# Optimization experiments

Measured on AMD Instinct MI355X. Metric: run time of the kernel, lower is better.

## Reference

```python
import jax, jax.numpy as jnp
import numpy as np

D = 128          # hidden_dim
H = 4            # num attention heads (torch default nhead=4 in this module)
DH = D // H
NA = 4096        # author nodes
NP = 100000      # paper nodes
EAP = 500000     # author->paper edges
EPA = 500000     # paper->author edges
DFF = 2048       # TransformerEncoderLayer FFN dim (torch default)
OUT = 16
IN_A = 128
IN_P = 256
EPS = 1e-5


def layer_norm(x, g, b):
    mu = jnp.mean(x, -1, keepdims=True)
    var = jnp.mean((x - mu) ** 2, -1, keepdims=True)
    return (x - mu) / jnp.sqrt(var + EPS) * g + b


def scatter_mean(vals, idx, n):
    # torch_scatter 'mean': empty segments yield 0
    s = jax.ops.segment_sum(vals, idx, num_segments=n)
    c = jax.ops.segment_sum(jnp.ones((vals.shape[0], 1), vals.dtype), idx, num_segments=n)
    return s / jnp.maximum(c, 1.0)


def metapath_layer(x_src, x_dst, src, dst, Wv, bv, Wo, bo, g, b):
    # nn.MultiheadAttention applied per-edge with seq_len=1 (query/key/value are
    # [1, E, D]); softmax over a single key is identically 1, so the attention
    # output is exactly out_proj(v_proj(x_src[src])) -- q/k projections have no
    # effect on the output (and zero gradient).
    v = x_src[src] @ Wv.T + bv            # [E, D] gather + value projection
    attn = v @ Wo.T + bo                  # output projection
    agg = scatter_mean(attn, dst, x_dst.shape[0])
    return layer_norm(agg + x_dst, g, b)


def fusion_layer(x, Wqkv, bqkv, Wo, bo, W1, b1, W2, b2, g1, bt1, g2, bt2):
    # torch TransformerEncoderLayer defaults: post-norm, relu, batch_first=False,
    # so x: [S=NA (seq), M (batch = #metapaths), D].
    S, M, _ = x.shape
    qkv = x @ Wqkv.T + bqkv               # [S, M, 3D]
    q, k, v = jnp.split(qkv, 3, axis=-1)
    q = q.reshape(S, M, H, DH)
    k = k.reshape(S, M, H, DH)
    v = v.reshape(S, M, H, DH)
    scores = jnp.einsum('smhd,tmhd->mhst', q, k) / np.float32(np.sqrt(DH))
    a = jax.nn.softmax(scores, axis=-1)
    ctx = jnp.einsum('mhst,tmhd->smhd', a, v).reshape(S, M, D)
    x = layer_norm(x + ctx @ Wo.T + bo, g1, bt1)
    ff = jax.nn.relu(x @ W1.T + b1) @ W2.T + b2
    return layer_norm(x + ff, g2, bt2)


def setup_inputs() -> dict:
    key = jax.random.key(0)
    ks = iter(jax.random.split(key, 64))
    def nrm(shape, scale=0.02):
        return jax.random.normal(next(ks), shape, dtype=jnp.float32) * scale
    inp = {
        'x_author': jax.random.normal(next(ks), (NA, IN_A), dtype=jnp.float32),
        'x_paper': jax.random.normal(next(ks), (NP, IN_P), dtype=jnp.float32),
        'src_ap': jax.random.randint(next(ks), (EAP,), 0, NA),
        'dst_ap': jax.random.randint(next(ks), (EAP,), 0, NP),
        'src_pa': jax.random.randint(next(ks), (EPA,), 0, NP),
        'dst_pa': jax.random.randint(next(ks), (EPA,), 0, NA),
        'pa_W': nrm((D, IN_A)), 'pa_b': nrm((D,)),
        'pp_W': nrm((D, IN_P)), 'pp_b': nrm((D,)),
        'f_Wqkv': nrm((3 * D, D)), 'f_bqkv': nrm((3 * D,)),
        'f_Wo': nrm((D, D)), 'f_bo': nrm((D,)),
        'f_W1': nrm((DFF, D)), 'f_b1': nrm((DFF,)),
        'f_W2': nrm((D, DFF)), 'f_b2': nrm((D,)),
        'f_g1': jnp.ones((D,), jnp.float32), 'f_bt1': jnp.zeros((D,), jnp.float32),
        'f_g2': jnp.ones((D,), jnp.float32), 'f_bt2': jnp.zeros((D,), jnp.float32),
        'cls_W': nrm((OUT, D)), 'cls_b': nrm((OUT,)),
    }
    for i in range(3):
        inp[f'l{i}_Wv'] = nrm((D, D)); inp[f'l{i}_bv'] = nrm((D,))
        inp[f'l{i}_Wo'] = nrm((D, D)); inp[f'l{i}_bo'] = nrm((D,))
        inp[f'l{i}_g'] = jnp.ones((D,), jnp.float32); inp[f'l{i}_b'] = jnp.zeros((D,), jnp.float32)
    return inp


def reference(x_author, x_paper, src_ap, dst_ap, src_pa, dst_pa,
              pa_W, pa_b, pp_W, pp_b,
              f_Wqkv, f_bqkv, f_Wo, f_bo, f_W1, f_b1, f_W2, f_b2,
              f_g1, f_bt1, f_g2, f_bt2, cls_W, cls_b,
              l0_Wv, l0_bv, l0_Wo, l0_bo, l0_g, l0_b,
              l1_Wv, l1_bv, l1_Wo, l1_bo, l1_g, l1_b,
              l2_Wv, l2_bv, l2_Wo, l2_bo, l2_g, l2_b):
    # project node features to hidden_dim
    ha = x_author @ pa_W.T + pa_b         # [NA, D]
    hp = x_paper @ pp_W.T + pp_b          # [NP, D]
    # metapath 0: paper -> author (one MetapathLayer)
    mp0 = metapath_layer(hp, ha, src_pa, dst_pa, l0_Wv, l0_bv, l0_Wo, l0_bo, l0_g, l0_b)
    # metapath 1: author -> paper -> author (two MetapathLayers)
    t = metapath_layer(ha, hp, src_ap, dst_ap, l1_Wv, l1_bv, l1_Wo, l1_bo, l1_g, l1_b)
    mp1 = metapath_layer(t, ha, src_pa, dst_pa, l2_Wv, l2_bv, l2_Wo, l2_bo, l2_g, l2_b)
    stacked = jnp.stack([mp0, mp1], axis=1)   # [NA, 2, D]
    fused = fusion_layer(stacked, f_Wqkv, f_bqkv, f_Wo, f_bo,
                         f_W1, f_b1, f_W2, f_b2,
                         f_g1, f_bt1, f_g2, f_bt2).mean(axis=1)
    return fused @ cls_W.T + cls_b            # [NA, OUT]
```

## Files before the change

### kernel.cpp

```cpp
#include <hip/hip_runtime.h>
#include <math.h>

constexpr int NA = 4096, NP = 100000, E_AP = 500000, E_PA = 500000;
constexpr int D = 128, DFF = 2048, NOUT = 16, IN_A = 128, IN_P = 256;

typedef __attribute__((ext_vector_type(8))) short bf16x8;
typedef __attribute__((ext_vector_type(4))) float f32x4;
typedef unsigned int u32;

__device__ __forceinline__ ushort f2b(float x) {
    union { float f; unsigned u; } v; v.f = x;
    unsigned r = v.u + 0x7fff + ((v.u >> 16) & 1);
    return (ushort)(r >> 16);
}
__device__ __forceinline__ float b2f(ushort h) {
    union { unsigned u; float f; } v; v.u = (unsigned)h << 16;
    return v.f;
}
__device__ __forceinline__ u32 fbits(float x) {
    union { float f; u32 u; } v; v.f = x; return v.u;
}

__device__ __forceinline__ bf16x8 cvtfrag(float4 a, float4 b) {
    union { u32 w[4]; bf16x8 v; } r;
    asm("v_cvt_pk_bf16_f32 %0, %1, %2" : "=v"(r.w[0]) : "v"(a.x), "v"(a.y));
    asm("v_cvt_pk_bf16_f32 %0, %1, %2" : "=v"(r.w[1]) : "v"(a.z), "v"(a.w));
    asm("v_cvt_pk_bf16_f32 %0, %1, %2" : "=v"(r.w[2]) : "v"(b.x), "v"(b.y));
    asm("v_cvt_pk_bf16_f32 %0, %1, %2" : "=v"(r.w[3]) : "v"(b.z), "v"(b.w));
    return r.v;
}

#define GLL(gp, lp) __builtin_amdgcn_global_load_lds( \
    (const __attribute__((address_space(1))) u32*)(gp), \
    (__attribute__((address_space(3))) u32*)(lp), 16, 0, 0)

__global__ __launch_bounds__(256) void gemm_bf16(
    const ushort* __restrict__ Abf, const float* __restrict__ Af32, int lda,
    const ushort* __restrict__ B, int ldb,
    const float* __restrict__ bias,
    float* __restrict__ outf, ushort* __restrict__ outh, int ldc,
    int M, int N, int K, int act)
{
    __shared__ ushort sA[64 * 32];
    __shared__ ushort sB[128 * 32];
    const int wave = threadIdx.x >> 6;
    const int lane = threadIdx.x & 63;
    const int l16 = lane & 15, quad = lane >> 4;
    const int row0 = blockIdx.y * 64;
    const int col0 = blockIdx.x * 128;
    const int wr0 = (wave >> 1) * 32, wc0 = (wave & 1) * 64;
    const int nz = gridDim.z;
    const int ksub = K / nz;
    const int kbeg = blockIdx.z * ksub, kend = kbeg + ksub;

    f32x4 acc[2][4] = {};

    const int sc = lane >> 4, sr = lane & 15;
    const int arow = min(row0 + wave * 16 + sr, M - 1);
    const float*  ap  = Af32 ? Af32 + (long)arow * lda + sc * 8 : nullptr;
    const ushort* abp = Abf  ? Abf  + (long)arow * lda + sc * 8 : nullptr;
    const ushort* bp0 = B + (long)(col0 + (wave * 2) * 16 + sr) * ldb + sc * 8;
    const ushort* bp1 = B + (long)(col0 + (wave * 2 + 1) * 16 + sr) * ldb + sc * 8;

    for (int k0 = kbeg; k0 < kend; k0 += 32) {
        if (k0 != kbeg) __syncthreads();
        if (Af32) {
            float4 f0 = *(const float4*)(ap + k0);
            float4 f1 = *(const float4*)(ap + k0 + 4);
            *(bf16x8*)(sA + wave * 512 + lane * 8) = cvtfrag(f0, f1);
        } else {
            GLL(abp + k0, sA + wave * 512);
        }
        GLL(bp0 + k0, sB + (wave * 2) * 512);
        GLL(bp1 + k0, sB + (wave * 2 + 1) * 512);
        __syncthreads();

        bf16x8 af[2], bfr[4];
        #pragma unroll
        for (int i = 0; i < 2; ++i)
            af[i] = *(const bf16x8*)(sA + ((wr0 >> 4) + i) * 512 + lane * 8);
        #pragma unroll
        for (int j = 0; j < 4; ++j)
            bfr[j] = *(const bf16x8*)(sB + ((wc0 >> 4) + j) * 512 + lane * 8);
        #pragma unroll
        for (int i = 0; i < 2; ++i)
            #pragma unroll
            for (int j = 0; j < 4; ++j)
                acc[i][j] = __builtin_amdgcn_mfma_f32_16x16x32_bf16(
                    af[i], bfr[j], acc[i][j], 0, 0, 0);
    }

    #pragma unroll
    for (int i = 0; i < 2; ++i) {
        #pragma unroll
        for (int r = 0; r < 4; ++r) {
            int row = row0 + wr0 + i * 16 + quad * 4 + r;
            if (row >= M) continue;
            #pragma unroll
            for (int j = 0; j < 4; ++j) {
                int col = col0 + wc0 + j * 16 + l16;
                if (nz > 1) {
                    atomicAdd(&outf[(long)row * ldc + col], acc[i][j][r]);
                } else {
                    float v = acc[i][j][r] + (bias ? bias[col] : 0.f);
                    if (act) v = fmaxf(v, 0.f);
                    if (outf) outf[(long)row * ldc + col] = v;
                    if (outh) outh[(long)row * ldc + col] = f2b(v);
                }
            }
        }
    }
}

__global__ __launch_bounds__(256) void fuse_weights(
    const float* __restrict__ Wv0, const float* __restrict__ bv0,
    const float* __restrict__ Wo0, const float* __restrict__ bo0,
    const float* __restrict__ Wv1, const float* __restrict__ bv1,
    const float* __restrict__ Wo1, const float* __restrict__ bo1,
    const float* __restrict__ Wv2, const float* __restrict__ bv2,
    const float* __restrict__ Wo2, const float* __restrict__ bo2,
    ushort* __restrict__ Wfb, float* __restrict__ beff)
{
    int blk = blockIdx.x;
    if (blk >= 192) {
        int l = blk - 192;
        const float* bv = l == 0 ? bv0 : (l == 1 ? bv1 : bv2);
        const float* Wo = l == 0 ? Wo0 : (l == 1 ? Wo1 : Wo2);
        const float* bo = l == 0 ? bo0 : (l == 1 ? bo1 : bo2);
        if (threadIdx.x < 128) {
            int r = threadIdx.x;
            float acc = bo[r];
            #pragma unroll 8
            for (int j = 0; j < 128; ++j) acc += Wo[r * 128 + j] * bv[j];
            beff[l * 128 + r] = acc;
        }
        return;
    }
    int l = blk >> 6;
    const float* Wv = l == 0 ? Wv0 : (l == 1 ? Wv1 : Wv2);
    const float* Wo = l == 0 ? Wo0 : (l == 1 ? Wo1 : Wo2);
    int r = (blk & 63) * 2 + (threadIdx.x >> 7);
    int c = threadIdx.x & 127;
    float acc = 0.f;
    #pragma unroll 8
    for (int j = 0; j < 128; ++j)
        acc += Wo[r * 128 + j] * Wv[j * 128 + c];
    Wfb[l * 16384 + r * 128 + c] = f2b(acc);
}

__global__ void hist_kernel(const int* __restrict__ dst, int* __restrict__ cnt, int E)
{
    int e = blockIdx.x * 256 + threadIdx.x;
    if (e < E) atomicAdd(&cnt[dst[e]], 1);
}

__global__ __launch_bounds__(256) void scan_local(
    const int* __restrict__ in, int* __restrict__ out,
    int* __restrict__ bsum, int n)
{
    __shared__ int wsum[4];
    int t = threadIdx.x;
    int base = blockIdx.x * 1024 + t * 4;
    int v0 = (base + 0 < n) ? in[base + 0] : 0;
    int v1 = (base + 1 < n) ? in[base + 1] : 0;
    int v2 = (base + 2 < n) ? in[base + 2] : 0;
    int v3 = (base + 3 < n) ? in[base + 3] : 0;
    int tsum = v0 + v1 + v2 + v3;
    int lane = t & 63;
    int x = tsum;
    #pragma unroll
    for (int o = 1; o < 64; o <<= 1) {
        int y = __shfl_up(x, o, 64);
        if (lane >= o) x += y;
    }
    int wid = t >> 6;
    if (lane == 63) wsum[wid] = x;
    __syncthreads();
    int woff = 0;
    #pragma unroll
    for (int ww = 0; ww < 3; ++ww) if (ww < wid) woff += wsum[ww];
    int excl = x - tsum + woff;
    if (base + 0 < n) out[base + 0] = excl;
    if (base + 1 < n) out[base + 1] = excl + v0;
    if (base + 2 < n) out[base + 2] = excl + v0 + v1;
    if (base + 3 < n) out[base + 3] = excl + v0 + v1 + v2;
    if (bsum && t == 255) bsum[blockIdx.x] = excl + tsum;
}

__global__ void scan_add(int* __restrict__ off, const int* __restrict__ bofs, int n)
{
    int i = blockIdx.x * 256 + threadIdx.x;
    if (i < n) off[i] += bofs[i >> 10];
}

__global__ void copy_int_kernel(const int* __restrict__ a, int* __restrict__ b, int n)
{
    int i = blockIdx.x * 256 + threadIdx.x;
    if (i < n) b[i] = a[i];
}

__global__ void fill_csr_kernel(const int* __restrict__ src, const int* __restrict__ dst,
                                int* __restrict__ cur, int* __restrict__ esrc, int E)
{
    int e = blockIdx.x * 256 + threadIdx.x;
    if (e >= E) return;
    int slot = atomicAdd(&cur[dst[e]], 1);
    esrc[slot] = src[e];
}

__global__ __launch_bounds__(256) void gather_mean(
    const ushort* __restrict__ z, const int* __restrict__ off,
    const int* __restrict__ cnt, const int* __restrict__ esrc,
    ushort* __restrict__ outh, int R)
{
    int grp = threadIdx.x >> 5;
    int tg  = threadIdx.x & 31;
    int row = blockIdx.x * 8 + grp;
    if (row >= R) return;
    int e0 = off[row], deg = cnt[row];
    int eend = e0 + deg;
    float a0 = 0.f, a1 = 0.f, a2 = 0.f, a3 = 0.f;
    int e = e0;
    for (; e + 4 <= eend; e += 4) {
        int s0 = esrc[e], s1 = esrc[e + 1], s2 = esrc[e + 2], s3 = esrc[e + 3];
        ushort4 v0 = ((const ushort4*)(z + (long)s0 * 128))[tg];
        ushort4 v1 = ((const ushort4*)(z + (long)s1 * 128))[tg];
        ushort4 v2 = ((const ushort4*)(z + (long)s2 * 128))[tg];
        ushort4 v3 = ((const ushort4*)(z + (long)s3 * 128))[tg];
        a0 += b2f(v0.x) + b2f(v1.x) + b2f(v2.x) + b2f(v3.x);
        a1 += b2f(v0.y) + b2f(v1.y) + b2f(v2.y) + b2f(v3.y);
        a2 += b2f(v0.z) + b2f(v1.z) + b2f(v2.z) + b2f(v3.z);
        a3 += b2f(v0.w) + b2f(v1.w) + b2f(v2.w) + b2f(v3.w);
    }
    for (; e < eend; ++e) {
        int s = esrc[e];
        ushort4 v = ((const ushort4*)(z + (long)s * 128))[tg];
        a0 += b2f(v.x); a1 += b2f(v.y); a2 += b2f(v.z); a3 += b2f(v.w);
    }
    float inv = 1.f / fmaxf((float)deg, 1.f);
    ushort4 h4 = {f2b(a0 * inv), f2b(a1 * inv), f2b(a2 * inv), f2b(a3 * inv)};
    ((ushort4*)(outh + (long)row * 128))[tg] = h4;
}

__global__ __launch_bounds__(256) void gather_mean_ln(
    const ushort* __restrict__ z, const int* __restrict__ off,
    const int* __restrict__ cnt, const int* __restrict__ esrc,
    const ushort* __restrict__ base, const float* __restrict__ g,
    const float* __restrict__ b, ushort* __restrict__ outh, int R)
{
    int grp = threadIdx.x >> 5;
    int tg  = threadIdx.x & 31;
    int row = blockIdx.x * 8 + grp;
    if (row >= R) return;
    int e0 = off[row], deg = cnt[row];
    int eend = e0 + deg;
    float a0 = 0.f, a1 = 0.f, a2 = 0.f, a3 = 0.f;
    int e = e0;
    for (; e + 4 <= eend; e += 4) {
        int s0 = esrc[e], s1 = esrc[e + 1], s2 = esrc[e + 2], s3 = esrc[e + 3];
        ushort4 v0 = ((const ushort4*)(z + (long)s0 * 128))[tg];
        ushort4 v1 = ((const ushort4*)(z + (long)s1 * 128))[tg];
        ushort4 v2 = ((const ushort4*)(z + (long)s2 * 128))[tg];
        ushort4 v3 = ((const ushort4*)(z + (long)s3 * 128))[tg];
        a0 += b2f(v0.x) + b2f(v1.x) + b2f(v2.x) + b2f(v3.x);
        a1 += b2f(v0.y) + b2f(v1.y) + b2f(v2.y) + b2f(v3.y);
        a2 += b2f(v0.z) + b2f(v1.z) + b2f(v2.z) + b2f(v3.z);
        a3 += b2f(v0.w) + b2f(v1.w) + b2f(v2.w) + b2f(v3.w);
    }
    for (; e < eend; ++e) {
        int s = esrc[e];
        ushort4 v = ((const ushort4*)(z + (long)s * 128))[tg];
        a0 += b2f(v.x); a1 += b2f(v.y); a2 += b2f(v.z); a3 += b2f(v.w);
    }
    float inv = 1.f / fmaxf((float)deg, 1.f);
    ushort4 bs = ((const ushort4*)(base + (long)row * 128))[tg];
    float x0 = a0 * inv + b2f(bs.x), x1 = a1 * inv + b2f(bs.y);
    float x2 = a2 * inv + b2f(bs.z), x3 = a3 * inv + b2f(bs.w);
    float s1 = x0 + x1 + x2 + x3;
    #pragma unroll
    for (int o = 1; o < 32; o <<= 1) s1 += __shfl_xor(s1, o, 64);
    float mu = s1 * (1.f / 128.f);
    float d0 = x0 - mu, d1 = x1 - mu, d2 = x2 - mu, d3 = x3 - mu;
    float s2 = d0 * d0 + d1 * d1 + d2 * d2 + d3 * d3;
    #pragma unroll
    for (int o = 1; o < 32; o <<= 1) s2 += __shfl_xor(s2, o, 64);
    float rstd = rsqrtf(s2 * (1.f / 128.f) + 1e-5f);
    float4 gv = ((const float4*)g)[tg];
    float4 bv = ((const float4*)b)[tg];
    ushort4 h4;
    h4.x = f2b(d0 * rstd * gv.x + bv.x);
    h4.y = f2b(d1 * rstd * gv.y + bv.y);
    h4.z = f2b(d2 * rstd * gv.z + bv.z);
    h4.w = f2b(d3 * rstd * gv.w + bv.w);
    ((ushort4*)(outh + (long)row * 128))[tg] = h4;
}

__global__ __launch_bounds__(128) void mean_add_ln(
    const float* __restrict__ a, const float* __restrict__ bias,
    const float* __restrict__ basef, const ushort* __restrict__ baseh,
    const float* __restrict__ g, const float* __restrict__ b,
    float* __restrict__ outf, ushort* __restrict__ outh, int out_ld, int R)
{
    int row = blockIdx.x;
    if (row >= R) return;
    int d = threadIdx.x;
    float x = a[(long)row * 128 + d];
    if (bias) x += bias[d];
    if (basef) x += basef[(long)row * 128 + d];
    if (baseh) x += b2f(baseh[(long)row * 128 + d]);

    __shared__ float red[4];
    float s = x;
    #pragma unroll
    for (int o = 32; o >= 1; o >>= 1) s += __shfl_xor(s, o, 64);
    if ((d & 63) == 0) red[d >> 6] = s;
    __syncthreads();
    float mu = (red[0] + red[1]) * (1.f / 128.f);
    float dx = x - mu;
    float s2 = dx * dx;
    #pragma unroll
    for (int o = 32; o >= 1; o >>= 1) s2 += __shfl_xor(s2, o, 64);
    if ((d & 63) == 0) red[2 + (d >> 6)] = s2;
    __syncthreads();
    float var = (red[2] + red[3]) * (1.f / 128.f);
    float v = dx * rsqrtf(var + 1e-5f) * g[d] + b[d];
    if (outf) outf[(long)row * out_ld + d] = v;
    if (outh) outh[(long)row * out_ld + d] = f2b(v);
}

struct CvtArgs { const float* in[6]; ushort* out[6]; int n4[6]; };
__global__ void cvt_multi(CvtArgs a)
{
    int j = blockIdx.y;
    int i = blockIdx.x * 256 + threadIdx.x;
    if (i >= a.n4[j]) return;
    float4 v = ((const float4*)a.in[j])[i];
    ushort4 o;
    o.x = f2b(v.x); o.y = f2b(v.y); o.z = f2b(v.z); o.w = f2b(v.w);
    ((ushort4*)a.out[j])[i] = o;
}

__global__ __launch_bounds__(256) void flash_attn(
    const ushort* __restrict__ qkvb,
    float* __restrict__ opart, float* __restrict__ lpart_g)
{
    const int qt = blockIdx.x;
    const int mh = blockIdx.y;
    const int ks = blockIdx.z;
    const int m = mh >> 2, h = mh & 3;
    const int wave = threadIdx.x >> 6;
    const int lane = threadIdx.x & 63;
    const int l16 = lane & 15, quad = lane >> 4;

    __shared__ ushort sK[2][64 * 40];
    __shared__ u32    sV[2][32 * 32];
    __shared__ u32    sP[4][16 * 32];

    const int q0 = qt * 64 + wave * 16;
    const float qs = 0.17677669529663687f * 1.4426950408889634f;
    bf16x8 qf;
    {
        bf16x8 qraw = *(const bf16x8*)(qkvb + ((long)(q0 + l16) * 2 + m) * 384 + h * 32 + quad * 8);
        #pragma unroll
        for (int j = 0; j < 8; ++j)
            qf[j] = (short)f2b(b2f((ushort)qraw[j]) * qs);
    }

    f32x4 oacc0 = {0.f, 0.f, 0.f, 0.f};
    f32x4 oacc1 = {0.f, 0.f, 0.f, 0.f};
    float lp = 0.f;

    const int skey = threadIdx.x >> 2, sseg = threadIdx.x & 3;
    const int vkp  = threadIdx.x & 31, vdc  = (threadIdx.x >> 5) * 4;
    const int kbeg = ks * (NA / 4);
    const ushort* kbase = qkvb + ((long)((kbeg + skey) * 2 + m)) * 384 + 128 + h * 32 + sseg * 8;
    const ushort* vbase = qkvb + ((long)((kbeg + vkp * 2) * 2 + m)) * 384 + 256 + h * 32 + vdc;
    const int kwo = skey * 40 + sseg * 8;
    int vwo[4];
    #pragma unroll
    for (int i = 0; i < 4; ++i)
        vwo[i] = (vdc + i) * 32 + ((((vkp >> 2) ^ ((vdc + i) & 7)) << 2) | (vkp & 3));

    bf16x8 kreg = *(const bf16x8*)(kbase);
    ushort4 v0r = *(const ushort4*)(vbase);
    ushort4 v1r = *(const ushort4*)(vbase + 768);
    *(bf16x8*)(&sK[0][kwo]) = kreg;
    sV[0][vwo[0]] = (u32)v0r.x | ((u32)v1r.x << 16);
    sV[0][vwo[1]] = (u32)v0r.y | ((u32)v1r.y << 16);
    sV[0][vwo[2]] = (u32)v0r.z | ((u32)v1r.z << 16);
    sV[0][vwo[3]] = (u32)v0r.w | ((u32)v1r.w << 16);
    __syncthreads();

    int cur = 0;
    for (int kt = 0; kt < 16; ++kt) {
        const bool more = (kt + 1) < 16;
        if (more) {
            long off = (long)(kt + 1) * 64 * 768;
            kreg = *(const bf16x8*)(kbase + off);
            v0r  = *(const ushort4*)(vbase + off);
            v1r  = *(const ushort4*)(vbase + off + 768);
        }

        #pragma unroll
        for (int t = 0; t < 4; ++t) {
            bf16x8 kf = *(const bf16x8*)(&sK[cur][(t * 16 + l16) * 40 + quad * 8]);
            f32x4 s = {0.f, 0.f, 0.f, 0.f};
            s = __builtin_amdgcn_mfma_f32_16x16x32_bf16(kf, qf, s, 0, 0, 0);
            float p0 = exp2f(s[0]), p1 = exp2f(s[1]);
            float p2 = exp2f(s[2]), p3 = exp2f(s[3]);
            lp += (p0 + p1) + (p2 + p3);
            u32 lo = __builtin_amdgcn_perm(fbits(p1), fbits(p0), 0x07060302u);
            u32 hi = __builtin_amdgcn_perm(fbits(p3), fbits(p2), 0x07060302u);
            u32* dst = &sP[wave][l16 * 32 +
                                 ((((t * 2 + (quad >> 1)) ^ (l16 & 7)) << 2) | ((quad & 1) * 2))];
            dst[0] = lo; dst[1] = hi;
        }
        #pragma unroll
        for (int c = 0; c < 2; ++c) {
            const int gp = ((c * 4 + quad) ^ (l16 & 7)) << 2;
            bf16x8 pf  = *(const bf16x8*)(&sP[wave][l16 * 32 + gp]);
            bf16x8 vf0 = *(const bf16x8*)(&sV[cur][l16 * 32 + gp]);
            bf16x8 vf1 = *(const bf16x8*)(&sV[cur][(16 + l16) * 32 + gp]);
            oacc0 = __builtin_amdgcn_mfma_f32_16x16x32_bf16(pf, vf0, oacc0, 0, 0, 0);
            oacc1 = __builtin_amdgcn_mfma_f32_16x16x32_bf16(pf, vf1, oacc1, 0, 0, 0);
        }

        if (more) {
            const int nxt = cur ^ 1;
            *(bf16x8*)(&sK[nxt][kwo]) = kreg;
            sV[nxt][vwo[0]] = (u32)v0r.x | ((u32)v1r.x << 16);
            sV[nxt][vwo[1]] = (u32)v0r.y | ((u32)v1r.y << 16);
            sV[nxt][vwo[2]] = (u32)v0r.z | ((u32)v1r.z << 16);
            sV[nxt][vwo[3]] = (u32)v0r.w | ((u32)v1r.w << 16);
            __syncthreads();
            cur = nxt;
        }
    }

    lp += __shfl_xor(lp, 16, 64);
    lp += __shfl_xor(lp, 32, 64);
    if (quad == 0)
        lpart_g[(long)(mh * 4 + ks) * NA + q0 + l16] = lp;

    #pragma unroll
    for (int r = 0; r < 4; ++r) {
        int qr = q0 + quad * 4 + r;
        long ob = ((long)(mh * 4 + ks) * NA + qr) * 32;
        opart[ob + l16]      = oacc0[r];
        opart[ob + 16 + l16] = oacc1[r];
    }
}

__global__ void attn_combine(const float* __restrict__ opart,
                             const float* __restrict__ lpart,
                             ushort* __restrict__ ctxb)
{
    int idx = blockIdx.x * 256 + threadIdx.x;
    int d = idx & 31;
    int row = idx >> 5;
    int mh = row >> 12, qrow = row & 4095;
    float o = 0.f, l = 0.f;
    #pragma unroll
    for (int ks = 0; ks < 4; ++ks) {
        long rb = (long)(mh * 4 + ks) * NA + qrow;
        o += opart[rb * 32 + d];
        l += lpart[rb];
    }
    int m = mh >> 2, h = mh & 3;
    ctxb[((long)qrow * 2 + m) * 128 + h * 32 + d] = f2b(o / l);
}

__global__ void classify_kernel(const float* __restrict__ x2,
                                const float* __restrict__ Wc,
                                const float* __restrict__ bc,
                                float* __restrict__ out)
{
    int idx = blockIdx.x * 256 + threadIdx.x;
    int a2 = idx >> 4, o = idx & 15;
    const float* r0 = x2 + (long)(a2 * 2) * 128;
    const float* r1 = r0 + 128;
    const float* w = Wc + o * 128;
    float acc = bc[o];
    #pragma unroll 4
    for (int dd = 0; dd < 128; ++dd) acc += 0.5f * (r0[dd] + r1[dd]) * w[dd];
    out[idx] = acc;
}

static void bgemm(hipStream_t st, const ushort* Abf, const float* Af32, int lda,
                  const ushort* B, int ldb,
                  const float* bias, float* outf, ushort* outh, int ldc,
                  int M, int N, int K, int act = 0, int ksplit = 1)
{
    dim3 grid(N / 128, (M + 63) / 64, ksplit);
    gemm_bf16<<<grid, 256, 0, st>>>(Abf, Af32, lda, B, ldb, bias, outf, outh,
                                    ldc, M, N, K, act);
}

static void build_csr(hipStream_t st, const int* src, const int* dst, int E, int n,
                      int* cnt, int* off, int* cur, int* bsum, int* esrc)
{
    hipMemsetAsync(cnt, 0, (size_t)n * 4, st);
    hist_kernel<<<(E + 255) / 256, 256, 0, st>>>(dst, cnt, E);
    int nb = (n + 1023) / 1024;
    scan_local<<<nb, 256, 0, st>>>(cnt, off, bsum, n);
    scan_local<<<1, 256, 0, st>>>(bsum, bsum, nullptr, nb);
    scan_add<<<(n + 255) / 256, 256, 0, st>>>(off, bsum, n);
    copy_int_kernel<<<(n + 255) / 256, 256, 0, st>>>(off, cur, n);
    fill_csr_kernel<<<(E + 255) / 256, 256, 0, st>>>(src, dst, cur, esrc, E);
}

extern "C" void kernel_launch(void* const* d_in, const int* in_sizes, int n_in,
                              void* d_out, int out_size, void* d_ws, size_t ws_size,
                              hipStream_t stream)
{
    const float* x_author = (const float*)d_in[0];
    const float* x_paper  = (const float*)d_in[1];
    const int*   src_ap   = (const int*)d_in[2];
    const int*   dst_ap   = (const int*)d_in[3];
    const int*   src_pa   = (const int*)d_in[4];
    const int*   dst_pa   = (const int*)d_in[5];
    const float* pa_W = (const float*)d_in[6];   const float* pa_b = (const float*)d_in[7];
    const float* pp_W = (const float*)d_in[8];   const float* pp_b = (const float*)d_in[9];
    const float* f_Wqkv = (const float*)d_in[10]; const float* f_bqkv = (const float*)d_in[11];
    const float* f_Wo = (const float*)d_in[12];  const float* f_bo = (const float*)d_in[13];
    const float* f_W1 = (const float*)d_in[14];  const float* f_b1 = (const float*)d_in[15];
    const float* f_W2 = (const float*)d_in[16];  const float* f_b2 = (const float*)d_in[17];
    const float* f_g1 = (const float*)d_in[18];  const float* f_bt1 = (const float*)d_in[19];
    const float* f_g2 = (const float*)d_in[20];  const float* f_bt2 = (const float*)d_in[21];
    const float* cls_W = (const float*)d_in[22]; const float* cls_b = (const float*)d_in[23];
    const float* l0_Wv = (const float*)d_in[24]; const float* l0_bv = (const float*)d_in[25];
    const float* l0_Wo = (const float*)d_in[26]; const float* l0_bo = (const float*)d_in[27];
    const float* l0_g  = (const float*)d_in[28]; const float* l0_b  = (const float*)d_in[29];
    const float* l1_Wv = (const float*)d_in[30]; const float* l1_bv = (const float*)d_in[31];
    const float* l1_Wo = (const float*)d_in[32]; const float* l1_bo = (const float*)d_in[33];
    const float* l1_g  = (const float*)d_in[34]; const float* l1_b  = (const float*)d_in[35];
    const float* l2_Wv = (const float*)d_in[36]; const float* l2_bv = (const float*)d_in[37];
    const float* l2_Wo = (const float*)d_in[38]; const float* l2_bo = (const float*)d_in[39];
    const float* l2_g  = (const float*)d_in[40]; const float* l2_b  = (const float*)d_in[41];

    uint8_t* w = (uint8_t*)d_ws;
    ushort* TB  = (ushort*)(w + 0);
    ushort* FF  = (ushort*)(w + 26214400);
    float*  OPART = (float*)(w + 26214400);
    float*  LPART = (float*)(w + 43515904);
    ushort* HPB = (ushort*)(w + 61440000);
    ushort* ZB  = (ushort*)(w + 87040000);
    uint8_t* p2 = w + 102400000;
    ushort* QKVB = (ushort*)(p2 + 0);
    ushort* CTXB = (ushort*)(p2 + 6291456);
    float*  TMP  = (float*)(p2 + 8388608);
    float*  X1   = (float*)(p2 + 12582912);
    ushort* X1B  = (ushort*)(p2 + 16777216);
    float*  TMP2 = (float*)(p2 + 18874368);
    float*  X2   = (float*)(p2 + 23068672);
    uint8_t* tail = p2 + 27262976;
    float*  STKF  = (float*)(tail + 0);
    ushort* STKB  = (ushort*)(tail + 4194304);
    ushort* HAB   = (ushort*)(tail + 6291456);
    ushort* GMA   = (ushort*)(tail + 7340032);
    ushort* WFB   = (ushort*)(tail + 8388608);
    ushort* PAWB  = (ushort*)(tail + 8486912);
    ushort* PPWB  = (ushort*)(tail + 8519680);
    ushort* WQKVB = (ushort*)(tail + 8585216);
    ushort* WOB   = (ushort*)(tail + 8683520);
    ushort* W1B   = (ushort*)(tail + 8716288);
    ushort* W2B   = (ushort*)(tail + 9240576);
    float*  BEFF  = (float*)(tail + 9764864);
    int*   CNT_A  = (int*)(tail + 9766400);
    int*   OFF_A  = (int*)(tail + 9782784);
    int*   CUR_A  = (int*)(tail + 9799168);
    int*   CNT_P  = (int*)(tail + 9815552);
    int*   OFF_P  = (int*)(tail + 10215552);
    int*   CUR_P  = (int*)(tail + 10615552);
    int*   ESRC_PA= (int*)(tail + 11015552);
    int*   ESRC_AP= (int*)(tail + 13015552);
    int*   BSUM_A = (int*)(tail + 15015552);
    int*   BSUM_P = (int*)(tail + 15016576);
    float* TMPA   = (float*)(tail + 15017984);

    CvtArgs ca;
    ca.in[0] = pa_W;   ca.out[0] = PAWB;  ca.n4[0] = D * IN_A / 4;
    ca.in[1] = pp_W;   ca.out[1] = PPWB;  ca.n4[1] = D * IN_P / 4;
    ca.in[2] = f_Wqkv; ca.out[2] = WQKVB; ca.n4[2] = 3 * D * D / 4;
    ca.in[3] = f_Wo;   ca.out[3] = WOB;   ca.n4[3] = D * D / 4;
    ca.in[4] = f_W1;   ca.out[4] = W1B;   ca.n4[4] = DFF * D / 4;
    ca.in[5] = f_W2;   ca.out[5] = W2B;   ca.n4[5] = D * DFF / 4;
    cvt_multi<<<dim3((DFF * D / 4 + 255) / 256, 6), 256, 0, stream>>>(ca);

    fuse_weights<<<195, 256, 0, stream>>>(l0_Wv, l0_bv, l0_Wo, l0_bo,
                                          l1_Wv, l1_bv, l1_Wo, l1_bo,
                                          l2_Wv, l2_bv, l2_Wo, l2_bo, WFB, BEFF);

    build_csr(stream, src_pa, dst_pa, E_PA, NA, CNT_A, OFF_A, CUR_A, BSUM_A, ESRC_PA);
    build_csr(stream, src_ap, dst_ap, E_AP, NP, CNT_P, OFF_P, CUR_P, BSUM_P, ESRC_AP);

    bgemm(stream, nullptr, x_author, IN_A, PAWB, IN_A, pa_b, nullptr, HAB, D, NA, D, IN_A);
    bgemm(stream, nullptr, x_paper,  IN_P, PPWB, IN_P, pp_b, nullptr, HPB, D, NP, D, IN_P);

    gather_mean<<<(NA + 7) / 8, 256, 0, stream>>>(HPB, OFF_A, CNT_A, ESRC_PA, GMA, NA);
    hipMemsetAsync(TMPA, 0, (size_t)NA * D * 4, stream);
    bgemm(stream, GMA, nullptr, D, WFB, D, nullptr, TMPA, nullptr, D, NA, D, D, 0, 4);
    mean_add_ln<<<NA, 128, 0, stream>>>(TMPA, BEFF, nullptr, HAB, l0_g, l0_b,
                                        nullptr, STKB, 256, NA);

    bgemm(stream, HAB, nullptr, D, WFB + 16384, D, BEFF + 128, nullptr, ZB, D, NA, D, D);
    gather_mean_ln<<<(NP + 7) / 8, 256, 0, stream>>>(
        ZB, OFF_P, CNT_P, ESRC_AP, HPB, l1_g, l1_b, TB, NP);

    gather_mean<<<(NA + 7) / 8, 256, 0, stream>>>(TB, OFF_A, CNT_A, ESRC_PA, GMA, NA);
    hipMemsetAsync(TMPA, 0, (size_t)NA * D * 4, stream);
    bgemm(stream, GMA, nullptr, D, WFB + 32768, D, nullptr, TMPA, nullptr, D, NA, D, D, 0, 4);
    mean_add_ln<<<NA, 128, 0, stream>>>(TMPA, BEFF + 256, nullptr, HAB, l2_g, l2_b,
                                        nullptr, STKB + 128, 256, NA);

    bgemm(stream, STKB, nullptr, D, WQKVB, D, f_bqkv, nullptr, QKVB, 3 * D, 2 * NA, 3 * D, D);
    flash_attn<<<dim3(NA / 64, 8, 4), 256, 0, stream>>>(QKVB, OPART, LPART);
    attn_combine<<<8 * NA * 32 / 256, 256, 0, stream>>>(OPART, LPART, CTXB);

    hipMemsetAsync(TMP, 0, (size_t)2 * NA * D * 4, stream);
    bgemm(stream, CTXB, nullptr, D, WOB, D, nullptr, TMP, nullptr, D, 2 * NA, D, D, 0, 4);
    mean_add_ln<<<2 * NA, 128, 0, stream>>>(TMP, f_bo, nullptr, STKB, f_g1, f_bt1,
                                            X1, X1B, 128, 2 * NA);

    bgemm(stream, X1B, nullptr, D, W1B, D, f_b1, nullptr, FF, DFF, 2 * NA, DFF, D, 1);
    hipMemsetAsync(TMP2, 0, (size_t)2 * NA * D * 4, stream);
    bgemm(stream, FF, nullptr, DFF, W2B, DFF, nullptr, TMP2, nullptr, D, 2 * NA, D, DFF, 0, 8);
    mean_add_ln<<<2 * NA, 128, 0, stream>>>(TMP2, f_b2, X1, nullptr, f_g2, f_bt2,
                                            X2, nullptr, 128, 2 * NA);

    classify_kernel<<<(NA * NOUT) / 256, 256, 0, stream>>>(X2, cls_W, cls_b, (float*)d_out);
}
```

Before: 729.1 us.

## Stage 128-wide K chunks in padded LDS and drop split-K for small GEMMs

The GEMM kernel now loads a 128-element K slab per iteration into padded LDS (1040-byte rows), so there are four MFMA sub-steps per barrier instead of one. The A tile is loaded with direct vector loads, one row per lane. The three K=128 GEMMs that used split-K with atomics and a memset now run as single-pass launches with the bias fused in. This cuts barriers, memsets and atomic traffic. The cost is fewer blocks for the small GEMMs, and the kernel now requires K per split to be a multiple of 128.

```diff
diff --git a/kernel.cpp b/kernel.cpp
--- a/kernel.cpp
+++ b/kernel.cpp
@@ -41,60 +41,78 @@
     float* __restrict__ outf, ushort* __restrict__ outh, int ldc,
     int M, int N, int K, int act)
 {
-    __shared__ ushort sA[64 * 32];
-    __shared__ ushort sB[128 * 32];
+    __shared__ uint8_t lds[(16 + 32) * 1040];
+    uint8_t* sAb = lds;
+    uint8_t* sBb = lds + 16 * 1040;
+
     const int wave = threadIdx.x >> 6;
     const int lane = threadIdx.x & 63;
     const int l16 = lane & 15, quad = lane >> 4;
     const int row0 = blockIdx.y * 64;
     const int col0 = blockIdx.x * 128;
-    const int wr0 = (wave >> 1) * 32, wc0 = (wave & 1) * 64;
+    const int wrg = (wave >> 1) * 2;
+    const int wc0 = (wave & 1) * 64;
     const int nz = gridDim.z;
     const int ksub = K / nz;
-    const int kbeg = blockIdx.z * ksub, kend = kbeg + ksub;
+    const int kbeg = blockIdx.z * ksub;
+    const int kgrps = ksub >> 7;
 
     f32x4 acc[2][4] = {};
 
-    const int sc = lane >> 4, sr = lane & 15;
-    const int arow = min(row0 + wave * 16 + sr, M - 1);
-    const float*  ap  = Af32 ? Af32 + (long)arow * lda + sc * 8 : nullptr;
-    const ushort* abp = Abf  ? Abf  + (long)arow * lda + sc * 8 : nullptr;
-    const ushort* bp0 = B + (long)(col0 + (wave * 2) * 16 + sr) * ldb + sc * 8;
-    const ushort* bp1 = B + (long)(col0 + (wave * 2 + 1) * 16 + sr) * ldb + sc * 8;
-
-    for (int k0 = kbeg; k0 < kend; k0 += 32) {
-        if (k0 != kbeg) __syncthreads();
+    const int sr = lane & 15, sc = lane >> 4;
+    const int arow = min(row0 + lane, M - 1);
+    const int ag = lane >> 4;
+    uint8_t* adst = sAb + (ag * 4 + wave) * 1040 + sr * 16;
+
+    for (int grp = 0; grp < kgrps; ++grp) {
+        const int kg = kbeg + grp * 128;
+        if (grp) __syncthreads();
+        #pragma unroll
+        for (int gg = 0; gg < 2; ++gg) {
+            int g = wave * 2 + gg;
+            const ushort* bp = B + (long)(col0 + g * 16 + sr) * ldb + kg + sc * 8;
+            #pragma unroll
+            for (int s = 0; s < 4; ++s)
+                GLL(bp + s * 32, sBb + (g * 4 + s) * 1040);
+        }
         if (Af32) {
-            float4 f0 = *(const float4*)(ap + k0);
-            float4 f1 = *(const float4*)(ap + k0 + 4);
-            *(bf16x8*)(sA + wave * 512 + lane * 8) = cvtfrag(f0, f1);
+            const float* ap = Af32 + (long)arow * lda + kg + wave * 32;
+            #pragma unroll
+            for (int q = 0; q < 4; ++q) {
+                float4 f0 = *(const float4*)(ap + q * 8);
+                float4 f1 = *(const float4*)(ap + q * 8 + 4);
+                *(bf16x8*)(adst + q * 256) = cvtfrag(f0, f1);
+            }
         } else {
-            GLL(abp + k0, sA + wave * 512);
-        }
-        GLL(bp0 + k0, sB + (wave * 2) * 512);
-        GLL(bp1 + k0, sB + (wave * 2 + 1) * 512);
+            const ushort* ap = Abf + (long)arow * lda + kg + wave * 32;
+            #pragma unroll
+            for (int q = 0; q < 4; ++q)
+                *(bf16x8*)(adst + q * 256) = *(const bf16x8*)(ap + q * 8);
+        }
         __syncthreads();
-
-        bf16x8 af[2], bfr[4];
         #pragma unroll
-        for (int i = 0; i < 2; ++i)
-            af[i] = *(const bf16x8*)(sA + ((wr0 >> 4) + i) * 512 + lane * 8);
-        #pragma unroll
-        for (int j = 0; j < 4; ++j)
-            bfr[j] = *(const bf16x8*)(sB + ((wc0 >> 4) + j) * 512 + lane * 8);
-        #pragma unroll
-        for (int i = 0; i < 2; ++i)
+        for (int s = 0; s < 4; ++s) {
+            bf16x8 af[2], bfr[4];
+            #pragma unroll
+            for (int i = 0; i < 2; ++i)
+                af[i] = *(const bf16x8*)(sAb + ((wrg + i) * 4 + s) * 1040 + lane * 16);
             #pragma unroll
             for (int j = 0; j < 4; ++j)
-                acc[i][j] = __builtin_amdgcn_mfma_f32_16x16x32_bf16(
-                    af[i], bfr[j], acc[i][j], 0, 0, 0);
+                bfr[j] = *(const bf16x8*)(sBb + (((wc0 >> 4) + j) * 4 + s) * 1040 + lane * 16);
+            #pragma unroll
+            for (int i = 0; i < 2; ++i)
+                #pragma unroll
+                for (int j = 0; j < 4; ++j)
+                    acc[i][j] = __builtin_amdgcn_mfma_f32_16x16x32_bf16(
+                        af[i], bfr[j], acc[i][j], 0, 0, 0);
+        }
     }
 
     #pragma unroll
     for (int i = 0; i < 2; ++i) {
         #pragma unroll
         for (int r = 0; r < 4; ++r) {
-            int row = row0 + wr0 + i * 16 + quad * 4 + r;
+            int row = row0 + wrg * 16 + i * 16 + quad * 4 + r;
             if (row >= M) continue;
             #pragma unroll
             for (int j = 0; j < 4; ++j) {
@@ -598,9 +616,8 @@
     bgemm(stream, nullptr, x_paper,  IN_P, PPWB, IN_P, pp_b, nullptr, HPB, D, NP, D, IN_P);
 
     gather_mean<<<(NA + 7) / 8, 256, 0, stream>>>(HPB, OFF_A, CNT_A, ESRC_PA, GMA, NA);
-    hipMemsetAsync(TMPA, 0, (size_t)NA * D * 4, stream);
-    bgemm(stream, GMA, nullptr, D, WFB, D, nullptr, TMPA, nullptr, D, NA, D, D, 0, 4);
-    mean_add_ln<<<NA, 128, 0, stream>>>(TMPA, BEFF, nullptr, HAB, l0_g, l0_b,
+    bgemm(stream, GMA, nullptr, D, WFB, D, BEFF, TMPA, nullptr, D, NA, D, D);
+    mean_add_ln<<<NA, 128, 0, stream>>>(TMPA, nullptr, nullptr, HAB, l0_g, l0_b,
                                         nullptr, STKB, 256, NA);
 
     bgemm(stream, HAB, nullptr, D, WFB + 16384, D, BEFF + 128, nullptr, ZB, D, NA, D, D);
@@ -608,18 +625,16 @@
         ZB, OFF_P, CNT_P, ESRC_AP, HPB, l1_g, l1_b, TB, NP);
 
     gather_mean<<<(NA + 7) / 8, 256, 0, stream>>>(TB, OFF_A, CNT_A, ESRC_PA, GMA, NA);
-    hipMemsetAsync(TMPA, 0, (size_t)NA * D * 4, stream);
-    bgemm(stream, GMA, nullptr, D, WFB + 32768, D, nullptr, TMPA, nullptr, D, NA, D, D, 0, 4);
-    mean_add_ln<<<NA, 128, 0, stream>>>(TMPA, BEFF + 256, nullptr, HAB, l2_g, l2_b,
+    bgemm(stream, GMA, nullptr, D, WFB + 32768, D, BEFF + 256, TMPA, nullptr, D, NA, D, D);
+    mean_add_ln<<<NA, 128, 0, stream>>>(TMPA, nullptr, nullptr, HAB, l2_g, l2_b,
                                         nullptr, STKB + 128, 256, NA);
 
     bgemm(stream, STKB, nullptr, D, WQKVB, D, f_bqkv, nullptr, QKVB, 3 * D, 2 * NA, 3 * D, D);
     flash_attn<<<dim3(NA / 64, 8, 4), 256, 0, stream>>>(QKVB, OPART, LPART);
     attn_combine<<<8 * NA * 32 / 256, 256, 0, stream>>>(OPART, LPART, CTXB);
 
-    hipMemsetAsync(TMP, 0, (size_t)2 * NA * D * 4, stream);
-    bgemm(stream, CTXB, nullptr, D, WOB, D, nullptr, TMP, nullptr, D, 2 * NA, D, D, 0, 4);
-    mean_add_ln<<<2 * NA, 128, 0, stream>>>(TMP, f_bo, nullptr, STKB, f_g1, f_bt1,
+    bgemm(stream, CTXB, nullptr, D, WOB, D, f_bo, TMP, nullptr, D, 2 * NA, D, D);
+    mean_add_ln<<<2 * NA, 128, 0, stream>>>(TMP, nullptr, nullptr, STKB, f_g1, f_bt1,
                                             X1, X1B, 128, 2 * NA);
 
     bgemm(stream, X1B, nullptr, D, W1B, D, f_b1, nullptr, FF, DFF, 2 * NA, DFF, D, 1);
```

Measured after the change: 706.6 us. 3.1% less time.
